# Performance work log

Measured on AMD Instinct MI355X. Metric: run time of the kernel, lower is better.

Reference implementation:

```python
import jax, jax.numpy as jnp
import numpy as np
from jax import lax

EPS = 1e-5

def conv3x3(x, w):
    # x: [B,C,H,W], w: [O,C,3,3]
    return lax.conv_general_dilated(x, w, (1, 1), ((1, 1), (1, 1)),
                                    dimension_numbers=("NCHW", "OIHW", "NCHW"))

def convbnrelu(x, w, bn):
    gamma, beta, mean, var = bn  # each [C]
    y = conv3x3(x, w)
    scale = (gamma / jnp.sqrt(var + EPS))[:, None, None]
    shift = (beta - mean * gamma / jnp.sqrt(var + EPS))[:, None, None]
    return jax.nn.relu(y * scale + shift)

def conv1x1(x, w, b):
    # w: [O,C,1,1], b: [O]
    return jnp.einsum("bchw,oc->bohw", x, w[:, :, 0, 0]) + b[:, None, None]

def pam(x, wb, bb, wc, bc, wd, bd, alpha, lfm=None):
    B, C, H, W = x.shape
    N = H * W
    q = conv1x1(x, wb, bb)
    k = conv1x1(x, wc, bc)
    v = conv1x1(x, wd, bd)
    if lfm is not None:  # VFAM: qkv flags all 1 -> multiply q, k, v
        q = q * lfm
        k = k * lfm
        v = v * lfm
    fb = q.reshape(B, -1, N).transpose(0, 2, 1)           # [B,N,Cq]
    fc = k.reshape(B, -1, N)                              # [B,Cq,N]
    attn = jax.nn.softmax(jnp.matmul(fb, fc), axis=-1)    # [B,N,N]
    fd = v.reshape(B, C, N)                               # [B,C,N]
    fe = jnp.matmul(fd, attn.transpose(0, 2, 1)).reshape(B, C, H, W)
    return alpha * fe + x

def cam(x, beta):
    B, C, H, W = x.shape
    N = H * W
    fa = x.reshape(B, C, N)
    attn = jnp.matmul(fa, fa.transpose(0, 2, 1))          # [B,C,C]
    attn = jnp.max(attn, axis=-1, keepdims=True) - attn
    attn = jax.nn.softmax(attn, axis=-1)
    fe = jnp.matmul(attn, fa).reshape(B, C, H, W)
    return beta * fe + x

def setup_inputs() -> dict:
    key = jax.random.key(0)
    ks = iter(jax.random.split(key, 64))
    B, Cin, H, W = 2, 2048, 64, 64
    Cmid = Cin // 4         # 512
    Cq = Cmid // 8          # 64
    nclass = 19

    def bn_pack(C):
        g = jnp.ones((C,)) + 0.1 * jax.random.normal(next(ks), (C,))
        b = 0.1 * jax.random.normal(next(ks), (C,))
        m = 0.1 * jax.random.normal(next(ks), (C,))
        v = jax.random.uniform(next(ks), (C,), minval=0.5, maxval=1.5)
        return jnp.stack([g, b, m, v])  # [4,C]

    def conv_w(O, I, kk):
        return jax.random.normal(next(ks), (O, I, kk, kk)) * (1.0 / np.sqrt(I * kk * kk))

    inp = {
        "x": jax.random.normal(next(ks), (B, Cin, H, W)),
        "loss_factor_map": jax.random.uniform(next(ks), (H, W)),
        "wp1": conv_w(Cmid, Cin, 3), "bnp1": bn_pack(Cmid),
        "wp2": conv_w(Cmid, Cmid, 3), "bnp2": bn_pack(Cmid),
        "wc1": conv_w(Cmid, Cin, 3), "bnc1": bn_pack(Cmid),
        "wc2": conv_w(Cmid, Cmid, 3), "bnc2": bn_pack(Cmid),
        "wv1": conv_w(Cmid, Cin, 3), "bnv1": bn_pack(Cmid),
        "wv2": conv_w(Cmid, Cmid, 3), "bnv2": bn_pack(Cmid),
        "pam_wb": conv_w(Cq, Cmid, 1), "pam_bb": jnp.zeros((Cq,)),
        "pam_wc": conv_w(Cq, Cmid, 1), "pam_bc": jnp.zeros((Cq,)),
        "pam_wd": conv_w(Cmid, Cmid, 1), "pam_bd": jnp.zeros((Cmid,)),
        "pam_alpha": 0.3 * jnp.ones((1,)),
        "cam_beta": 0.3 * jnp.ones((1,)),
        "vfam_wb": conv_w(Cq, Cmid, 1), "vfam_bb": jnp.zeros((Cq,)),
        "vfam_wc": conv_w(Cq, Cmid, 1), "vfam_bc": jnp.zeros((Cq,)),
        "vfam_wd": conv_w(Cmid, Cmid, 1), "vfam_bd": jnp.zeros((Cmid,)),
        "vfam_alpha": 0.3 * jnp.ones((1,)),
        "out_w": conv_w(nclass, Cmid, 1), "out_b": jnp.zeros((nclass,)),
        "p3_w": conv_w(nclass, Cmid, 1), "p3_b": jnp.zeros((nclass,)),
        "c3_w": conv_w(nclass, Cmid, 1), "c3_b": jnp.zeros((nclass,)),
    }
    return inp

def reference(x, loss_factor_map,
              wp1, bnp1, wp2, bnp2, wc1, bnc1, wc2, bnc2, wv1, bnv1, wv2, bnv2,
              pam_wb, pam_bb, pam_wc, pam_bc, pam_wd, pam_bd, pam_alpha,
              cam_beta,
              vfam_wb, vfam_bb, vfam_wc, vfam_bc, vfam_wd, vfam_bd, vfam_alpha,
              out_w, out_b, p3_w, p3_b, c3_w, c3_b):
    lfm = loss_factor_map[None, None, :, :]  # (1,1,H,W)
    # Position branch
    fp = convbnrelu(x, wp1, bnp1)
    fp = pam(fp, pam_wb, pam_bb, pam_wc, pam_bc, pam_wd, pam_bd, pam_alpha)
    fp = convbnrelu(fp, wp2, bnp2)
    # Channel branch
    fc = convbnrelu(x, wc1, bnc1)
    fc = cam(fc, cam_beta)
    fc = convbnrelu(fc, wc2, bnc2)
    # Visual-field branch (qkv_vfa_flag = [1,1,1])
    fv = convbnrelu(x, wv1, bnv1)
    fv = pam(fv, vfam_wb, vfam_bb, vfam_wc, vfam_bc, vfam_wd, vfam_bd, vfam_alpha, lfm=lfm)
    fv = convbnrelu(fv, wv2, bnv2)
    # Fusion + heads (Dropout in eval mode = identity)
    fusion = fp + fc + fv
    fusion_out = conv1x1(fusion, out_w, out_b)
    p_out = conv1x1(fp, p3_w, p3_b)
    c_out = conv1x1(fc, c3_w, c3_b)
    return (fusion_out, p_out, c_out)
```

## Files before the change

kernel.cpp:

```cpp
#include <hip/hip_runtime.h>

typedef unsigned short u16;
typedef short s16x8 __attribute__((ext_vector_type(8)));
typedef u16 u16x8 __attribute__((ext_vector_type(8)));
typedef u16 u16x4 __attribute__((ext_vector_type(4)));
typedef float f32x4 __attribute__((ext_vector_type(4)));

#define DEV __device__ __forceinline__

DEV float bf2f(u16 x) { unsigned v = ((unsigned)x) << 16; float f; __builtin_memcpy(&f, &v, 4); return f; }
DEV u16 f2bf(float f) { unsigned u; __builtin_memcpy(&u, &f, 4); u += 0x7FFFu + ((u >> 16) & 1u); return (u16)(u >> 16); }

DEV void gload16(const u16* g, u16* l) {
  __builtin_amdgcn_global_load_lds((const __attribute__((address_space(1))) void*)g,
                                   (__attribute__((address_space(3))) void*)l, 16, 0, 0);
}

__global__ void detect_dtype(const u16* __restrict__ x, int* __restrict__ flag) {
  int tid = threadIdx.x;
  float mx = 0.f;
  for (int i = tid; i < 4096; i += 256) mx = fmaxf(mx, fabsf(bf2f(x[i])));
  __shared__ float red[4];
  int wave = tid >> 6, lane = tid & 63;
  for (int off = 32; off; off >>= 1) mx = fmaxf(mx, __shfl_xor(mx, off));
  if (lane == 0) red[wave] = mx;
  __syncthreads();
  if (tid == 0) {
    mx = fmaxf(fmaxf(red[0], red[1]), fmaxf(red[2], red[3]));
    *flag = (mx > 1e4f) ? 1 : 0;
  }
}

__global__ void convert_in(const void* __restrict__ src, u16* __restrict__ dst, int n,
                           const int* __restrict__ flag) {
  int i = blockIdx.x * 256 + threadIdx.x;
  if (i >= n) return;
  if (*flag) dst[i] = f2bf(((const float*)src)[i]);
  else       dst[i] = ((const u16*)src)[i];
}

__global__ void bn_prep(const u16* __restrict__ cbn, float* __restrict__ out) {
  int w = blockIdx.x;
  const u16* bn = cbn + w * 2048;
  int c = threadIdx.x;
  float g = bf2f(bn[c]), be = bf2f(bn[512 + c]), m = bf2f(bn[1024 + c]), v = bf2f(bn[1536 + c]);
  float sc = g * rsqrtf(v + 1e-5f);
  out[w * 1024 + c] = sc;
  out[w * 1024 + 512 + c] = be - m * sc;
}

__global__ __launch_bounds__(256) void repack_w3(const u16* __restrict__ w, u16* __restrict__ wr,
                                                 int I, int Ishift) {
  size_t idx = ((size_t)blockIdx.x * 256 + threadIdx.x) * 8;
  int i0 = (int)(idx & (size_t)(I - 1));
  int t = (int)(idx >> Ishift);
  int o = t / 9, kk = t - o * 9;
  u16x8 v;
#pragma unroll
  for (int j = 0; j < 8; ++j) v[j] = w[((size_t)o * I + i0 + j) * 9 + kk];
  *(u16x8*)&wr[idx] = v;
}

__global__ __launch_bounds__(256) void pad_nchw(const u16* __restrict__ x, u16* __restrict__ xpad) {
  __shared__ u16 t[64][72];
  int c0 = blockIdx.x * 64, h = blockIdx.y, b = blockIdx.z;
  int tid = threadIdx.x;
#pragma unroll
  for (int i = 0; i < 2; ++i) {
    int idx = i * 256 + tid;
    int cc = idx >> 3, ww = (idx & 7) * 8;
    u16x8 v = *(const u16x8*)&x[(((size_t)(b * 2048 + c0 + cc) * 64) + h) * 64 + ww];
    *(u16x8*)&t[cc][ww] = v;
  }
  __syncthreads();
#pragma unroll
  for (int i = 0; i < 2; ++i) {
    int idx = i * 256 + tid;
    int ww = idx >> 3, cc = (idx & 7) * 8;
    u16x8 v;
#pragma unroll
    for (int j = 0; j < 8; ++j) v[j] = t[cc + j][ww];
    *(u16x8*)&xpad[(((size_t)b * 66 + h + 1) * 66 + ww + 1) * 2048 + c0 + cc] = v;
  }
}

__global__ __launch_bounds__(256) void transpose64(const u16* __restrict__ src, u16* __restrict__ dst,
                                                   int R, int C) {
  __shared__ u16 t[64][72];
  int r0 = blockIdx.x * 64, c0 = blockIdx.y * 64;
  const u16* s = src + (size_t)blockIdx.z * R * C;
  u16* d = dst + (size_t)blockIdx.z * R * C;
  int tid = threadIdx.x;
#pragma unroll
  for (int i = 0; i < 2; ++i) {
    int idx = i * 256 + tid;
    int rr = idx >> 3, cc = (idx & 7) * 8;
    u16x8 v = *(const u16x8*)&s[(size_t)(r0 + rr) * C + c0 + cc];
    *(u16x8*)&t[rr][cc] = v;
  }
  __syncthreads();
#pragma unroll
  for (int i = 0; i < 2; ++i) {
    int idx = i * 256 + tid;
    int cc = idx >> 3, rr = (idx & 7) * 8;
    u16x8 v;
#pragma unroll
    for (int j = 0; j < 8; ++j) v[j] = t[rr + j][cc];
    *(u16x8*)&d[(size_t)(c0 + cc) * R + r0 + rr] = v;
  }
}

struct GemmP {
  const u16* A; const u16* B;
  long aBatch, bBatch;
  int M, N, K;
  u16* out; long outBatch; int ldOut;
  const u16* bias;
  const u16* rowscale;
  const u16* residual; long resBatch; int ldRes;
  const u16* alphaPtr;
  float* outF; long outFBatch;
};

template <int BM, int BN, int EPI>
__global__ __launch_bounds__(256) void gemm_nt(GemmP p) {
  __shared__ u16 lA[BM * 32], lB[BN * 32];
  const int tid = threadIdx.x;
  const int bz = blockIdx.z;
  const int m0 = blockIdx.x * BM, n0 = blockIdx.y * BN;
  const u16* A = p.A + (size_t)bz * p.aBatch;
  const u16* Bp = p.B + (size_t)bz * p.bBatch;
  const int wave = tid >> 6, lane = tid & 63;
  const int quad = lane >> 4, r16 = lane & 15;
  const int wm = (wave >> 1) * (BM / 2), wn = (wave & 1) * (BN / 2);
  constexpr int TM = BM / 32, TN = BN / 32;
  f32x4 acc[TM][TN] = {};
  const int srow = tid >> 2, sch = (tid & 3) * 8;
  const int K = p.K;
  for (int k0 = 0; k0 < K; k0 += 32) {
    u16x8 ra[BM / 64], rb[BN / 64];
#pragma unroll
    for (int i = 0; i < BM / 64; ++i)
      ra[i] = *(const u16x8*)&A[(size_t)(m0 + i * 64 + srow) * K + k0 + sch];
#pragma unroll
    for (int i = 0; i < BN / 64; ++i)
      rb[i] = *(const u16x8*)&Bp[(size_t)(n0 + i * 64 + srow) * K + k0 + sch];
    __syncthreads();
#pragma unroll
    for (int i = 0; i < BM / 64; ++i) *(u16x8*)&lA[i * 2048 + tid * 8] = ra[i];
#pragma unroll
    for (int i = 0; i < BN / 64; ++i) *(u16x8*)&lB[i * 2048 + tid * 8] = rb[i];
    __syncthreads();
    s16x8 av[TM], bv[TN];
#pragma unroll
    for (int t = 0; t < TM; ++t) av[t] = *(const s16x8*)&lA[(wm + t * 16 + r16) * 32 + quad * 8];
#pragma unroll
    for (int t = 0; t < TN; ++t) bv[t] = *(const s16x8*)&lB[(wn + t * 16 + r16) * 32 + quad * 8];
#pragma unroll
    for (int i = 0; i < TM; ++i)
#pragma unroll
      for (int j = 0; j < TN; ++j)
        acc[i][j] = __builtin_amdgcn_mfma_f32_16x16x32_bf16(av[i], bv[j], acc[i][j], 0, 0, 0);
  }
  float alpha = 0.f;
  if (EPI == 3) alpha = bf2f(p.alphaPtr[0]);
#pragma unroll
  for (int i = 0; i < TM; ++i) {
#pragma unroll
    for (int j = 0; j < TN; ++j) {
      const int nn = n0 + wn + j * 16 + r16;
      float bia = 0.f;
      if ((EPI == 0 || EPI == 1) && p.bias) bia = bf2f(p.bias[nn]);
#pragma unroll
      for (int r = 0; r < 4; ++r) {
        const int mm = m0 + wm + i * 16 + quad * 4 + r;
        float v = acc[i][j][r];
        if (EPI == 0) {
          v += bia;
          if (p.rowscale) v *= bf2f(p.rowscale[mm]);
          p.out[(size_t)bz * p.outBatch + (size_t)mm * p.ldOut + nn] = f2bf(v);
        } else if (EPI == 1) {
          v += bia;
          if (p.rowscale) v *= bf2f(p.rowscale[mm]);
          p.out[(size_t)bz * p.outBatch + (size_t)nn * p.ldOut + mm] = f2bf(v);
        } else if (EPI == 2) {
          p.outF[(size_t)bz * p.outFBatch + (size_t)mm * p.ldOut + nn] = v;
        } else {
          float res = bf2f(p.residual[(size_t)bz * p.resBatch + (size_t)mm * p.ldRes + nn]);
          v = alpha * v + res;
          const int py = mm >> 6, px = mm & 63;
          p.out[(size_t)bz * p.outBatch + ((size_t)(py + 1) * 66 + (px + 1)) * p.ldOut + nn] = f2bf(v);
        }
      }
    }
  }
}

struct Conv3P {
  const u16* in[3];
  const u16* wr[3];
  u16* out[3];
  const float* bn;
};

template <int CIN>
__global__ __launch_bounds__(256) void conv3x3_k(Conv3P p) {
  __shared__ u16 lA[4096], lB[4096];
  const int tid = threadIdx.x;
  const int z = blockIdx.z, ci = z >> 1, b = z & 1;
  const int m0 = blockIdx.x * 128, n0 = blockIdx.y * 128;
  const u16* __restrict__ xin = p.in[ci];
  const u16* __restrict__ wr = p.wr[ci];
  const int wave = tid >> 6, lane = tid & 63;
  const int quad = lane >> 4, r16 = lane & 15;
  const int wm = (wave >> 1) * 64, wn = (wave & 1) * 64;
  f32x4 acc[4][4] = {};
  const int srow = tid >> 2, sch = (tid & 3) * 8;
  const int p0 = m0 + srow, p1 = p0 + 64;
  const size_t a0 = (((size_t)b * 66 + (p0 >> 6)) * 66 + (p0 & 63)) * CIN + sch;
  const size_t a1 = (((size_t)b * 66 + (p1 >> 6)) * 66 + (p1 & 63)) * CIN + sch;
  const size_t b0 = ((size_t)(n0 + srow) * 9) * CIN + sch;
  const size_t b1 = ((size_t)(n0 + 64 + srow) * 9) * CIN + sch;
  u16* la0 = &lA[wave * 512];
  u16* la1 = &lA[2048 + wave * 512];
  u16* lb0 = &lB[wave * 512];
  u16* lb1 = &lB[2048 + wave * 512];
  for (int kh = 0; kh < 3; ++kh) {
    for (int kw = 0; kw < 3; ++kw) {
      const size_t soff = ((size_t)kh * 66 + kw) * CIN;
      const size_t woff = (size_t)(kh * 3 + kw) * CIN;
      for (int c = 0; c < CIN; c += 32) {
        __syncthreads();
        gload16(&xin[a0 + soff + c], la0);
        gload16(&xin[a1 + soff + c], la1);
        gload16(&wr[b0 + woff + c], lb0);
        gload16(&wr[b1 + woff + c], lb1);
        __syncthreads();
        s16x8 av[4], bv[4];
#pragma unroll
        for (int t = 0; t < 4; ++t) av[t] = *(const s16x8*)&lA[(wm + t * 16 + r16) * 32 + quad * 8];
#pragma unroll
        for (int t = 0; t < 4; ++t) bv[t] = *(const s16x8*)&lB[(wn + t * 16 + r16) * 32 + quad * 8];
#pragma unroll
        for (int i = 0; i < 4; ++i)
#pragma unroll
          for (int j = 0; j < 4; ++j)
            acc[i][j] = __builtin_amdgcn_mfma_f32_16x16x32_bf16(av[i], bv[j], acc[i][j], 0, 0, 0);
      }
    }
  }
  u16* __restrict__ out = p.out[ci];
  const float* bnS = p.bn + ci * 1024;
#pragma unroll
  for (int i = 0; i < 4; ++i) {
#pragma unroll
    for (int j = 0; j < 4; ++j) {
      const int nn = n0 + wn + j * 16 + r16;
      const float s = bnS[nn], sh = bnS[512 + nn];
#pragma unroll
      for (int r = 0; r < 4; ++r) {
        const int mm = m0 + wm + i * 16 + quad * 4 + r;
        float v = fmaxf(acc[i][j][r] * s + sh, 0.f);
        out[((size_t)b * 4096 + mm) * 512 + nn] = f2bf(v);
      }
    }
  }
}

__global__ __launch_bounds__(256) void softmax4096(const float* __restrict__ S, u16* __restrict__ P) {
  int row = blockIdx.x, tid = threadIdx.x;
  const float* sr = S + (size_t)row * 4096;
  f32x4 v[4];
  float mx = -3.4e38f;
#pragma unroll
  for (int i = 0; i < 4; ++i) {
    v[i] = *(const f32x4*)&sr[(i * 256 + tid) * 4];
    mx = fmaxf(mx, fmaxf(fmaxf(v[i][0], v[i][1]), fmaxf(v[i][2], v[i][3])));
  }
  __shared__ float red[8];
  int wave = tid >> 6, lane = tid & 63;
  for (int off = 32; off; off >>= 1) mx = fmaxf(mx, __shfl_xor(mx, off));
  if (lane == 0) red[wave] = mx;
  __syncthreads();
  mx = fmaxf(fmaxf(red[0], red[1]), fmaxf(red[2], red[3]));
  float sum = 0.f;
#pragma unroll
  for (int i = 0; i < 4; ++i)
#pragma unroll
    for (int j = 0; j < 4; ++j) { float e = __expf(v[i][j] - mx); v[i][j] = e; sum += e; }
  for (int off = 32; off; off >>= 1) sum += __shfl_xor(sum, off);
  if (lane == 0) red[4 + wave] = sum;
  __syncthreads();
  sum = red[4] + red[5] + red[6] + red[7];
  float inv = 1.f / sum;
  u16* pr = P + (size_t)row * 4096;
#pragma unroll
  for (int i = 0; i < 4; ++i) {
    u16x4 ov;
#pragma unroll
    for (int j = 0; j < 4; ++j) ov[j] = f2bf(v[i][j] * inv);
    *(u16x4*)&pr[(i * 256 + tid) * 4] = ov;
  }
}

__global__ __launch_bounds__(256) void softmax_cam(const float* __restrict__ S, u16* __restrict__ P) {
  int row = blockIdx.x, tid = threadIdx.x;
  const float* sr = S + (size_t)row * 512;
  float a = sr[tid], b = sr[tid + 256];
  __shared__ float red[12];
  int wave = tid >> 6, lane = tid & 63;
  float mx = fmaxf(a, b);
  for (int off = 32; off; off >>= 1) mx = fmaxf(mx, __shfl_xor(mx, off));
  if (lane == 0) red[wave] = mx;
  __syncthreads();
  float M1 = fmaxf(fmaxf(red[0], red[1]), fmaxf(red[2], red[3]));
  float mn = fminf(a, b);
  for (int off = 32; off; off >>= 1) mn = fminf(mn, __shfl_xor(mn, off));
  if (lane == 0) red[4 + wave] = mn;
  __syncthreads();
  float m2 = M1 - fminf(fminf(red[4], red[5]), fminf(red[6], red[7]));
  float e0 = __expf((M1 - a) - m2), e1 = __expf((M1 - b) - m2);
  float sum = e0 + e1;
  for (int off = 32; off; off >>= 1) sum += __shfl_xor(sum, off);
  if (lane == 0) red[8 + wave] = sum;
  __syncthreads();
  sum = red[8] + red[9] + red[10] + red[11];
  float inv = 1.f / sum;
  P[(size_t)row * 512 + tid] = f2bf(e0 * inv);
  P[(size_t)row * 512 + tid + 256] = f2bf(e1 * inv);
}

__global__ __launch_bounds__(256) void final_out_k(const u16* __restrict__ fp2, const u16* __restrict__ fc2,
                                                   const u16* __restrict__ fv2,
                                                   const u16* ow, const u16* ob, const u16* pw,
                                                   const u16* pb, const u16* cw, const u16* cb,
                                                   void* __restrict__ out, const int* __restrict__ flag) {
  __shared__ float wl[19 * 512];
  int tid = threadIdx.x, which = blockIdx.y;
  const u16* W = which == 0 ? ow : which == 1 ? pw : cw;
  const u16* Bb = which == 0 ? ob : which == 1 ? pb : cb;
  for (int i = tid; i < 19 * 512; i += 256) wl[i] = bf2f(W[i]);
  __syncthreads();
  int pix = blockIdx.x * 256 + threadIdx.x;
  size_t rb = (size_t)pix * 512;
  float acc[19];
#pragma unroll
  for (int o = 0; o < 19; ++o) acc[o] = 0.f;
  for (int c = 0; c < 512; c += 8) {
    float xs[8];
    if (which == 0) {
      u16x8 a = *(const u16x8*)&fp2[rb + c];
      u16x8 d = *(const u16x8*)&fc2[rb + c];
      u16x8 e = *(const u16x8*)&fv2[rb + c];
#pragma unroll
      for (int j = 0; j < 8; ++j) xs[j] = bf2f(a[j]) + bf2f(d[j]) + bf2f(e[j]);
    } else {
      const u16* src = which == 1 ? fp2 : fc2;
      u16x8 a = *(const u16x8*)&src[rb + c];
#pragma unroll
      for (int j = 0; j < 8; ++j) xs[j] = bf2f(a[j]);
    }
#pragma unroll
    for (int o = 0; o < 19; ++o) {
      const float* wv = &wl[o * 512 + c];
#pragma unroll
      for (int j = 0; j < 8; ++j) acc[o] += xs[j] * wv[j];
    }
  }
  int b = pix >> 12, n = pix & 4095;
  const int isF32 = *flag;
#pragma unroll
  for (int o = 0; o < 19; ++o) {
    size_t idx = (size_t)which * 155648 + ((size_t)(b * 19 + o)) * 4096 + n;
    float v = acc[o] + bf2f(Bb[o]);
    if (isF32) ((float*)out)[idx] = v;
    else ((u16*)out)[idx] = f2bf(v);
  }
}

static const size_t OFF_XPAD  = 0;
static const size_t OFF_WR1A  = 35684352;
static const size_t OFF_WR1B  = 54558720;
static const size_t OFF_WR1C  = 73433088;
static const size_t OFF_ARENA = 92307456;
static const size_t OFF_S     = 0;
static const size_t OFF_P     = 67108864;
static const size_t OFF_ARENA2= 0;
static const size_t OFF_FP1   = 125861888;
static const size_t OFF_FC1   = 134250496;
static const size_t OFF_FV1   = 142639104;
static const size_t OFF_FC1T  = 151027712;
static const size_t OFF_QT    = 159416320;
static const size_t OFF_KT    = 160464896;
static const size_t OFF_VT    = 161513472;
static const size_t OFF_WRSA  = 151027712;
static const size_t OFF_WRSB  = 155746304;
static const size_t OFF_WRSC  = 161513472;
static const size_t OFF_PADP  = 169902080;
static const size_t OFF_PADC  = 178823168;
static const size_t OFF_PADV  = 187744256;
static const size_t OFF_FP2   = 125861888;
static const size_t OFF_FC2   = 134250496;
static const size_t OFF_FV2   = 142639104;
static const size_t OFF_SC    = 196665344;
static const size_t OFF_PC    = 198762496;
static const size_t OFF_BN    = 199811072;
static const size_t OFF_FLAG  = 199835648;
static const size_t OFF_SMALL = 199835904;
static const size_t SO_CBN    = 0;
static const size_t SO_PWB    = 12288;
static const size_t SO_PBB    = 45056;
static const size_t SO_PWC    = 45120;
static const size_t SO_PBC    = 77888;
static const size_t SO_PWD    = 77952;
static const size_t SO_PBD    = 340096;
static const size_t SO_PAL    = 340608;
static const size_t SO_CBETA  = 340624;
static const size_t SO_VWB    = 340640;
static const size_t SO_VBB    = 373408;
static const size_t SO_VWC    = 373472;
static const size_t SO_VBC    = 406240;
static const size_t SO_VWD    = 406304;
static const size_t SO_VBD    = 668448;
static const size_t SO_VAL    = 668960;
static const size_t SO_OW     = 668976;
static const size_t SO_OB     = 678704;
static const size_t SO_PW3    = 678736;
static const size_t SO_PB3    = 688464;
static const size_t SO_CW3    = 688496;
static const size_t SO_CB3    = 698224;
static const size_t SO_LFM    = 698256;
static const size_t SO_END    = 702352;
static const size_t WS_NEEDED = OFF_SMALL + SO_END * 2;

extern "C" void kernel_launch(void* const* d_in, const int* in_sizes, int n_in,
                              void* d_out, int out_size, void* d_ws, size_t ws_size,
                              hipStream_t stream) {
  if (ws_size < WS_NEEDED) return;
  (void)in_sizes; (void)n_in; (void)out_size;

  char* ws = (char*)d_ws;
  u16* xpad   = (u16*)(ws + OFF_XPAD);
  u16* wr1a   = (u16*)(ws + OFF_WR1A);
  u16* wr1b   = (u16*)(ws + OFF_WR1B);
  u16* wr1c   = (u16*)(ws + OFF_WR1C);
  u16* arena  = (u16*)(ws + OFF_ARENA);
  u16* arena2 = (u16*)(ws + OFF_ARENA2);
  float* S    = (float*)(ws + OFF_S);
  u16* P      = (u16*)(ws + OFF_P);
  u16* fp1    = (u16*)(ws + OFF_FP1);
  u16* fc1    = (u16*)(ws + OFF_FC1);
  u16* fv1    = (u16*)(ws + OFF_FV1);
  u16* fc1T   = (u16*)(ws + OFF_FC1T);
  u16* qt     = (u16*)(ws + OFF_QT);
  u16* kt     = (u16*)(ws + OFF_KT);
  u16* vT     = (u16*)(ws + OFF_VT);
  u16* wrsa   = (u16*)(ws + OFF_WRSA);
  u16* wrsb   = (u16*)(ws + OFF_WRSB);
  u16* wrsc   = (u16*)(ws + OFF_WRSC);
  u16* padP   = (u16*)(ws + OFF_PADP);
  u16* padC   = (u16*)(ws + OFF_PADC);
  u16* padV   = (u16*)(ws + OFF_PADV);
  u16* fp2    = (u16*)(ws + OFF_FP2);
  u16* fc2    = (u16*)(ws + OFF_FC2);
  u16* fv2    = (u16*)(ws + OFF_FV2);
  float* Sc   = (float*)(ws + OFF_SC);
  u16* Pc     = (u16*)(ws + OFF_PC);
  float* bnb  = (float*)(ws + OFF_BN);
  int* flag   = (int*)(ws + OFF_FLAG);
  u16* sm     = (u16*)(ws + OFF_SMALL);

  detect_dtype<<<1, 256, 0, stream>>>((const u16*)d_in[0], flag);
  auto cv = [&](int i, u16* dst, int n) {
    convert_in<<<(n + 255) / 256, 256, 0, stream>>>(d_in[i], dst, n, flag);
  };
  cv(3,  sm + SO_CBN + 0 * 2048, 2048);
  cv(7,  sm + SO_CBN + 1 * 2048, 2048);
  cv(11, sm + SO_CBN + 2 * 2048, 2048);
  cv(5,  sm + SO_CBN + 3 * 2048, 2048);
  cv(9,  sm + SO_CBN + 4 * 2048, 2048);
  cv(13, sm + SO_CBN + 5 * 2048, 2048);
  cv(14, sm + SO_PWB, 32768);  cv(15, sm + SO_PBB, 64);
  cv(16, sm + SO_PWC, 32768);  cv(17, sm + SO_PBC, 64);
  cv(18, sm + SO_PWD, 262144); cv(19, sm + SO_PBD, 512);
  cv(20, sm + SO_PAL, 1);      cv(21, sm + SO_CBETA, 1);
  cv(22, sm + SO_VWB, 32768);  cv(23, sm + SO_VBB, 64);
  cv(24, sm + SO_VWC, 32768);  cv(25, sm + SO_VBC, 64);
  cv(26, sm + SO_VWD, 262144); cv(27, sm + SO_VBD, 512);
  cv(28, sm + SO_VAL, 1);
  cv(29, sm + SO_OW, 9728);    cv(30, sm + SO_OB, 19);
  cv(31, sm + SO_PW3, 9728);   cv(32, sm + SO_PB3, 19);
  cv(33, sm + SO_CW3, 9728);   cv(34, sm + SO_CB3, 19);
  cv(1,  sm + SO_LFM, 4096);

  bn_prep<<<6, 512, 0, stream>>>(sm + SO_CBN, bnb);

  cv(0, arena, 16777216);
  hipMemsetAsync(xpad, 0, 35684352, stream);
  pad_nchw<<<dim3(32, 64, 2), 256, 0, stream>>>(arena, xpad);

  cv(2, arena, 9437184);
  repack_w3<<<4608, 256, 0, stream>>>(arena, wr1a, 2048, 11);
  cv(6, arena, 9437184);
  repack_w3<<<4608, 256, 0, stream>>>(arena, wr1b, 2048, 11);
  cv(10, arena, 9437184);
  repack_w3<<<4608, 256, 0, stream>>>(arena, wr1c, 2048, 11);
  {
    Conv3P c{};
    c.in[0] = xpad; c.in[1] = xpad; c.in[2] = xpad;
    c.wr[0] = wr1a; c.wr[1] = wr1b; c.wr[2] = wr1c;
    c.out[0] = fp1; c.out[1] = fc1; c.out[2] = fv1;
    c.bn = bnb;
    conv3x3_k<2048><<<dim3(32, 4, 6), 256, 0, stream>>>(c);
  }

  auto runPam = [&](const u16* src, const u16* wb, const u16* bb, const u16* wck, const u16* bck,
                    const u16* wd, const u16* bd, const u16* alphaP, const u16* rs, u16* padOut) {
    GemmP g{};
    g.A = src; g.aBatch = 2097152; g.B = wb; g.bBatch = 0; g.M = 4096; g.N = 64; g.K = 512;
    g.out = qt; g.outBatch = 262144; g.ldOut = 64; g.bias = bb; g.rowscale = rs;
    gemm_nt<64, 64, 0><<<dim3(64, 1, 2), 256, 0, stream>>>(g);
    g.B = wck; g.bias = bck; g.out = kt;
    gemm_nt<64, 64, 0><<<dim3(64, 1, 2), 256, 0, stream>>>(g);
    GemmP gv{};
    gv.A = src; gv.aBatch = 2097152; gv.B = wd; gv.bBatch = 0; gv.M = 4096; gv.N = 512; gv.K = 512;
    gv.out = vT; gv.outBatch = 2097152; gv.ldOut = 4096; gv.bias = bd; gv.rowscale = rs;
    gemm_nt<64, 128, 1><<<dim3(64, 4, 2), 256, 0, stream>>>(gv);
    hipMemsetAsync(padOut, 0, 8921088, stream);
    for (int b = 0; b < 2; ++b) {
      GemmP gs{};
      gs.A = qt + (size_t)b * 262144; gs.B = kt + (size_t)b * 262144;
      gs.M = 4096; gs.N = 4096; gs.K = 64;
      gs.outF = S; gs.outFBatch = 0; gs.ldOut = 4096;
      gemm_nt<128, 128, 2><<<dim3(32, 32, 1), 256, 0, stream>>>(gs);
      softmax4096<<<4096, 256, 0, stream>>>(S, P);
      GemmP gf{};
      gf.A = P; gf.aBatch = 0; gf.B = vT + (size_t)b * 2097152; gf.bBatch = 0;
      gf.M = 4096; gf.N = 512; gf.K = 4096;
      gf.out = padOut + (size_t)b * 2230272; gf.outBatch = 0; gf.ldOut = 512;
      gf.residual = src + (size_t)b * 2097152; gf.resBatch = 0; gf.ldRes = 512;
      gf.alphaPtr = alphaP;
      gemm_nt<64, 64, 3><<<dim3(64, 8, 1), 256, 0, stream>>>(gf);
    }
  };
  runPam(fp1, sm + SO_PWB, sm + SO_PBB, sm + SO_PWC, sm + SO_PBC, sm + SO_PWD, sm + SO_PBD,
         sm + SO_PAL, nullptr, padP);
  runPam(fv1, sm + SO_VWB, sm + SO_VBB, sm + SO_VWC, sm + SO_VBC, sm + SO_VWD, sm + SO_VBD,
         sm + SO_VAL, sm + SO_LFM, padV);

  transpose64<<<dim3(64, 8, 2), 256, 0, stream>>>(fc1, fc1T, 4096, 512);
  {
    GemmP g{};
    g.A = fc1T; g.aBatch = 2097152; g.B = fc1T; g.bBatch = 2097152;
    g.M = 512; g.N = 512; g.K = 4096;
    g.outF = Sc; g.outFBatch = 262144; g.ldOut = 512;
    gemm_nt<64, 64, 2><<<dim3(8, 8, 2), 256, 0, stream>>>(g);
  }
  softmax_cam<<<1024, 256, 0, stream>>>(Sc, Pc);
  hipMemsetAsync(padC, 0, 8921088, stream);
  {
    GemmP g{};
    g.A = fc1; g.aBatch = 2097152; g.B = Pc; g.bBatch = 262144;
    g.M = 4096; g.N = 512; g.K = 512;
    g.out = padC; g.outBatch = 2230272; g.ldOut = 512;
    g.residual = fc1; g.resBatch = 2097152; g.ldRes = 512;
    g.alphaPtr = sm + SO_CBETA;
    gemm_nt<128, 128, 3><<<dim3(32, 4, 2), 256, 0, stream>>>(g);
  }

  cv(4, arena2, 2359296);
  repack_w3<<<1152, 256, 0, stream>>>(arena2, wrsa, 512, 9);
  cv(8, arena2, 2359296);
  repack_w3<<<1152, 256, 0, stream>>>(arena2, wrsb, 512, 9);
  cv(12, arena2, 2359296);
  repack_w3<<<1152, 256, 0, stream>>>(arena2, wrsc, 512, 9);
  {
    Conv3P c{};
    c.in[0] = padP; c.in[1] = padC; c.in[2] = padV;
    c.wr[0] = wrsa; c.wr[1] = wrsb; c.wr[2] = wrsc;
    c.out[0] = fp2; c.out[1] = fc2; c.out[2] = fv2;
    c.bn = bnb + 3 * 1024;
    conv3x3_k<512><<<dim3(32, 4, 6), 256, 0, stream>>>(c);
  }

  final_out_k<<<dim3(32, 3), 256, 0, stream>>>(fp2, fc2, fv2, sm + SO_OW, sm + SO_OB,
                                               sm + SO_PW3, sm + SO_PB3, sm + SO_CW3, sm + SO_CB3,
                                               d_out, flag);
}
```

Baseline: 1.696 ms.

## Fuse dtype conversion into pad/repack, merge Q/K GEMMs, coalesce fp32 score stores

The input and conv-weight dtype conversion is folded into the pad and weight-repack kernels, which removes the separate convert passes and their arena round trips. The Q and K projection GEMMs are merged into one launch by splitting the z-grid. The fp32 score GEMM epilogue now stages results through LDS so it can write coalesced 16-byte rows, and the PAM output GEMM tile grows to 128x64. This adds per-kernel flag branches and more LDS traffic in the epilogue.

New measurement: 1.722 ms. About the same (+1.5%).

```diff
diff --git a/kernel.cpp b/kernel.cpp
--- a/kernel.cpp
+++ b/kernel.cpp
@@ -49,27 +49,45 @@
   out[w * 1024 + 512 + c] = be - m * sc;
 }
 
-__global__ __launch_bounds__(256) void repack_w3(const u16* __restrict__ w, u16* __restrict__ wr,
-                                                 int I, int Ishift) {
+__global__ __launch_bounds__(256) void repack_w3(const void* __restrict__ w, u16* __restrict__ wr,
+                                                 int I, int Ishift, const int* __restrict__ flag) {
+  const int isF = *flag;
   size_t idx = ((size_t)blockIdx.x * 256 + threadIdx.x) * 8;
   int i0 = (int)(idx & (size_t)(I - 1));
   int t = (int)(idx >> Ishift);
   int o = t / 9, kk = t - o * 9;
   u16x8 v;
-#pragma unroll
-  for (int j = 0; j < 8; ++j) v[j] = w[((size_t)o * I + i0 + j) * 9 + kk];
+  if (isF) {
+    const float* f = (const float*)w;
+#pragma unroll
+    for (int j = 0; j < 8; ++j) v[j] = f2bf(f[((size_t)o * I + i0 + j) * 9 + kk]);
+  } else {
+    const u16* bsrc = (const u16*)w;
+#pragma unroll
+    for (int j = 0; j < 8; ++j) v[j] = bsrc[((size_t)o * I + i0 + j) * 9 + kk];
+  }
   *(u16x8*)&wr[idx] = v;
 }
 
-__global__ __launch_bounds__(256) void pad_nchw(const u16* __restrict__ x, u16* __restrict__ xpad) {
+__global__ __launch_bounds__(256) void pad_nchw(const void* __restrict__ x, u16* __restrict__ xpad,
+                                                const int* __restrict__ flag) {
   __shared__ u16 t[64][72];
+  const int isF = *flag;
   int c0 = blockIdx.x * 64, h = blockIdx.y, b = blockIdx.z;
   int tid = threadIdx.x;
 #pragma unroll
   for (int i = 0; i < 2; ++i) {
     int idx = i * 256 + tid;
     int cc = idx >> 3, ww = (idx & 7) * 8;
-    u16x8 v = *(const u16x8*)&x[(((size_t)(b * 2048 + c0 + cc) * 64) + h) * 64 + ww];
+    size_t base = (((size_t)(b * 2048 + c0 + cc) * 64) + h) * 64 + ww;
+    u16x8 v;
+    if (isF) {
+      const float* fx = (const float*)x;
+#pragma unroll
+      for (int j = 0; j < 8; ++j) v[j] = f2bf(fx[base + j]);
+    } else {
+      v = *(const u16x8*)&((const u16*)x)[base];
+    }
     *(u16x8*)&t[cc][ww] = v;
   }
   __syncthreads();
@@ -120,16 +138,27 @@
   const u16* residual; long resBatch; int ldRes;
   const u16* alphaPtr;
   float* outF; long outFBatch;
+  const u16* B2; const u16* bias2; u16* out2;
 };
 
 template <int BM, int BN, int EPI>
 __global__ __launch_bounds__(256) void gemm_nt(GemmP p) {
-  __shared__ u16 lA[BM * 32], lB[BN * 32];
+  static_assert(EPI != 2 || BM >= BN, "EPI2 LDS bounce needs BM>=BN");
+  __shared__ __align__(16) u16 lsBuf[(BM + BN) * 32];
+  u16* lA = lsBuf;
+  u16* lB = lsBuf + BM * 32;
   const int tid = threadIdx.x;
-  const int bz = blockIdx.z;
+  int bz = blockIdx.z;
+  const u16* Bsel = p.B;
+  const u16* biasSel = p.bias;
+  u16* outSel = p.out;
+  if (EPI == 0 && p.out2) {
+    const int h = gridDim.z >> 1;
+    if (bz >= h) { bz -= h; Bsel = p.B2; biasSel = p.bias2; outSel = p.out2; }
+  }
   const int m0 = blockIdx.x * BM, n0 = blockIdx.y * BN;
   const u16* A = p.A + (size_t)bz * p.aBatch;
-  const u16* Bp = p.B + (size_t)bz * p.bBatch;
+  const u16* Bp = Bsel + (size_t)bz * p.bBatch;
   const int wave = tid >> 6, lane = tid & 63;
   const int quad = lane >> 4, r16 = lane & 15;
   const int wm = (wave >> 1) * (BM / 2), wn = (wave & 1) * (BN / 2);
@@ -162,6 +191,33 @@
       for (int j = 0; j < TN; ++j)
         acc[i][j] = __builtin_amdgcn_mfma_f32_16x16x32_bf16(av[i], bv[j], acc[i][j], 0, 0, 0);
   }
+  if constexpr (EPI == 2) {
+    float* lsF = (float*)lsBuf;
+#pragma unroll
+    for (int i = 0; i < TM; ++i) {
+      __syncthreads();
+#pragma unroll
+      for (int j = 0; j < TN; ++j) {
+        const int col = wn + j * 16 + r16;
+#pragma unroll
+        for (int r = 0; r < 4; ++r) {
+          const int rowL = (wave >> 1) * 16 + quad * 4 + r;
+          lsF[rowL * BN + col] = acc[i][j][r];
+        }
+      }
+      __syncthreads();
+      constexpr int PASSES = (32 * BN) / 1024;
+#pragma unroll
+      for (int pp = 0; pp < PASSES; ++pp) {
+        const int lin = (pp * 256 + tid) * 4;
+        const int rowL = lin / BN, col = lin & (BN - 1);
+        const int gm = m0 + (rowL >> 4) * (BM / 2) + i * 16 + (rowL & 15);
+        *(f32x4*)&p.outF[(size_t)bz * p.outFBatch + (size_t)gm * p.ldOut + (n0 + col)] =
+            *(const f32x4*)&lsF[lin];
+      }
+    }
+    return;
+  }
   float alpha = 0.f;
   if (EPI == 3) alpha = bf2f(p.alphaPtr[0]);
 #pragma unroll
@@ -170,7 +226,7 @@
     for (int j = 0; j < TN; ++j) {
       const int nn = n0 + wn + j * 16 + r16;
       float bia = 0.f;
-      if ((EPI == 0 || EPI == 1) && p.bias) bia = bf2f(p.bias[nn]);
+      if ((EPI == 0 || EPI == 1) && biasSel) bia = bf2f(biasSel[nn]);
 #pragma unroll
       for (int r = 0; r < 4; ++r) {
         const int mm = m0 + wm + i * 16 + quad * 4 + r;
@@ -178,13 +234,11 @@
         if (EPI == 0) {
           v += bia;
           if (p.rowscale) v *= bf2f(p.rowscale[mm]);
-          p.out[(size_t)bz * p.outBatch + (size_t)mm * p.ldOut + nn] = f2bf(v);
+          outSel[(size_t)bz * p.outBatch + (size_t)mm * p.ldOut + nn] = f2bf(v);
         } else if (EPI == 1) {
           v += bia;
           if (p.rowscale) v *= bf2f(p.rowscale[mm]);
           p.out[(size_t)bz * p.outBatch + (size_t)nn * p.ldOut + mm] = f2bf(v);
-        } else if (EPI == 2) {
-          p.outF[(size_t)bz * p.outFBatch + (size_t)mm * p.ldOut + nn] = v;
         } else {
           float res = bf2f(p.residual[(size_t)bz * p.resBatch + (size_t)mm * p.ldRes + nn]);
           v = alpha * v + res;
@@ -385,7 +439,6 @@
 static const size_t OFF_ARENA = 92307456;
 static const size_t OFF_S     = 0;
 static const size_t OFF_P     = 67108864;
-static const size_t OFF_ARENA2= 0;
 static const size_t OFF_FP1   = 125861888;
 static const size_t OFF_FC1   = 134250496;
 static const size_t OFF_FV1   = 142639104;
@@ -444,8 +497,6 @@
   u16* wr1a   = (u16*)(ws + OFF_WR1A);
   u16* wr1b   = (u16*)(ws + OFF_WR1B);
   u16* wr1c   = (u16*)(ws + OFF_WR1C);
-  u16* arena  = (u16*)(ws + OFF_ARENA);
-  u16* arena2 = (u16*)(ws + OFF_ARENA2);
   float* S    = (float*)(ws + OFF_S);
   u16* P      = (u16*)(ws + OFF_P);
   u16* fp1    = (u16*)(ws + OFF_FP1);
@@ -495,16 +546,12 @@
 
   bn_prep<<<6, 512, 0, stream>>>(sm + SO_CBN, bnb);
 
-  cv(0, arena, 16777216);
   hipMemsetAsync(xpad, 0, 35684352, stream);
-  pad_nchw<<<dim3(32, 64, 2), 256, 0, stream>>>(arena, xpad);
-
-  cv(2, arena, 9437184);
-  repack_w3<<<4608, 256, 0, stream>>>(arena, wr1a, 2048, 11);
-  cv(6, arena, 9437184);
-  repack_w3<<<4608, 256, 0, stream>>>(arena, wr1b, 2048, 11);
-  cv(10, arena, 9437184);
-  repack_w3<<<4608, 256, 0, stream>>>(arena, wr1c, 2048, 11);
+  pad_nchw<<<dim3(32, 64, 2), 256, 0, stream>>>(d_in[0], xpad, flag);
+
+  repack_w3<<<4608, 256, 0, stream>>>(d_in[2],  wr1a, 2048, 11, flag);
+  repack_w3<<<4608, 256, 0, stream>>>(d_in[6],  wr1b, 2048, 11, flag);
+  repack_w3<<<4608, 256, 0, stream>>>(d_in[10], wr1c, 2048, 11, flag);
   {
     Conv3P c{};
     c.in[0] = xpad; c.in[1] = xpad; c.in[2] = xpad;
@@ -519,9 +566,8 @@
     GemmP g{};
     g.A = src; g.aBatch = 2097152; g.B = wb; g.bBatch = 0; g.M = 4096; g.N = 64; g.K = 512;
     g.out = qt; g.outBatch = 262144; g.ldOut = 64; g.bias = bb; g.rowscale = rs;
-    gemm_nt<64, 64, 0><<<dim3(64, 1, 2), 256, 0, stream>>>(g);
-    g.B = wck; g.bias = bck; g.out = kt;
-    gemm_nt<64, 64, 0><<<dim3(64, 1, 2), 256, 0, stream>>>(g);
+    g.B2 = wck; g.bias2 = bck; g.out2 = kt;
+    gemm_nt<64, 64, 0><<<dim3(64, 1, 4), 256, 0, stream>>>(g);
     GemmP gv{};
     gv.A = src; gv.aBatch = 2097152; gv.B = wd; gv.bBatch = 0; gv.M = 4096; gv.N = 512; gv.K = 512;
     gv.out = vT; gv.outBatch = 2097152; gv.ldOut = 4096; gv.bias = bd; gv.rowscale = rs;
@@ -540,7 +586,7 @@
       gf.out = padOut + (size_t)b * 2230272; gf.outBatch = 0; gf.ldOut = 512;
       gf.residual = src + (size_t)b * 2097152; gf.resBatch = 0; gf.ldRes = 512;
       gf.alphaPtr = alphaP;
-      gemm_nt<64, 64, 3><<<dim3(64, 8, 1), 256, 0, stream>>>(gf);
+      gemm_nt<128, 64, 3><<<dim3(32, 8, 1), 256, 0, stream>>>(gf);
     }
   };
   runPam(fp1, sm + SO_PWB, sm + SO_PBB, sm + SO_PWC, sm + SO_PBC, sm + SO_PWD, sm + SO_PBD,
@@ -568,12 +614,9 @@
     gemm_nt<128, 128, 3><<<dim3(32, 4, 2), 256, 0, stream>>>(g);
   }
 
-  cv(4, arena2, 2359296);
-  repack_w3<<<1152, 256, 0, stream>>>(arena2, wrsa, 512, 9);
-  cv(8, arena2, 2359296);
-  repack_w3<<<1152, 256, 0, stream>>>(arena2, wrsb, 512, 9);
-  cv(12, arena2, 2359296);
-  repack_w3<<<1152, 256, 0, stream>>>(arena2, wrsc, 512, 9);
+  repack_w3<<<1152, 256, 0, stream>>>(d_in[4],  wrsa, 512, 9, flag);
+  repack_w3<<<1152, 256, 0, stream>>>(d_in[8],  wrsb, 512, 9, flag);
+  repack_w3<<<1152, 256, 0, stream>>>(d_in[12], wrsc, 512, 9, flag);
   {
     Conv3P c{};
     c.in[0] = padP; c.in[1] = padC; c.in[2] = padV;
```
